# Performance work log

Hardware: AMD Instinct MI355X
Metric: run time of the kernel (lower is better)

The kernel has to match this reference:

```python
import jax, jax.numpy as jnp
import numpy as np

NUM_USERS = 100000
NUM_FEATURES = 1024
FACTORS = 64
B = 16384
TOTAL_FEATS = 524288  # B * 32 avg features per (user,item) pair


def setup_inputs() -> dict:
    key = jax.random.key(0)
    k1, k2, k3, k4, k5, k6 = jax.random.split(key, 6)
    user = jax.random.randint(k1, (B,), 0, NUM_USERS)
    # flattened ragged uifm[user][item] feature lists: sample_idx maps each
    # gathered feature id back to its batch row
    sample_idx = jax.random.randint(k2, (TOTAL_FEATS,), 0, B)
    feat_idx = jax.random.randint(k3, (TOTAL_FEATS,), 0, NUM_FEATURES)
    H = jax.random.normal(k4, (NUM_USERS, FACTORS), dtype=jnp.float32)
    G = jax.random.normal(k5, (NUM_FEATURES, FACTORS), dtype=jnp.float32)
    K = jax.random.normal(k6, (NUM_USERS, NUM_FEATURES), dtype=jnp.float32)
    return {"user": user, "sample_idx": sample_idx, "feat_idx": feat_idx,
            "H": H, "G": G, "K": K}


def reference(user, sample_idx, feat_idx, H, G, K):
    h_u = H[user]                      # [B, factors]
    z_u = jnp.einsum('bf,nf->bn', h_u, G)  # [B, num_features]
    a_u = K[user] * z_u                # [B, num_features] feature affinities
    # ragged gather-sum over per-(user,item) feature lists, then batch sum
    vals = a_u[sample_idx, feat_idx]   # [TOTAL_FEATS]
    return jnp.sum(vals)
```

## Files before the change

kernel.cpp:

```cpp
#include <hip/hip_runtime.h>

#define N_TOTAL   524288
#define B_ROWS    16384
#define FACTORS   64
#define NFEAT     1024

#define BM 128
#define BF 128
#define LDS_PAD 132

__global__ void zero_out_kernel(float* out) {
    out[0] = 0.0f;
}

__global__ __launch_bounds__(256, 2) void dense_c_kernel(
    const int*   __restrict__ user,
    const float* __restrict__ H,
    const float* __restrict__ G,
    float*       __restrict__ C,
    float*       __restrict__ out)
{
    if (blockIdx.x == 0 && threadIdx.x == 0) out[0] = 0.0f;

    __shared__ float sHT[FACTORS * LDS_PAD];
    __shared__ float sGT[FACTORS * LDS_PAD];

    const int t  = threadIdx.x;
    const int bb = (int)(blockIdx.x >> 3) * BM;
    const int bf = (int)(blockIdx.x & 7)  * BF;

    for (int i = t; i < BM * (FACTORS / 4); i += 256) {
        const int row  = i >> 4;
        const int slot = i & 15;

        const int u = user[bb + row];
        const float4 h = *(const float4*)(H + (long)u * FACTORS + slot * 4);
        sHT[(slot * 4 + 0) * LDS_PAD + row] = h.x;
        sHT[(slot * 4 + 1) * LDS_PAD + row] = h.y;
        sHT[(slot * 4 + 2) * LDS_PAD + row] = h.z;
        sHT[(slot * 4 + 3) * LDS_PAD + row] = h.w;

        const float4 g = *(const float4*)(G + (long)(bf + row) * FACTORS + slot * 4);
        sGT[(slot * 4 + 0) * LDS_PAD + row] = g.x;
        sGT[(slot * 4 + 1) * LDS_PAD + row] = g.y;
        sGT[(slot * 4 + 2) * LDS_PAD + row] = g.z;
        sGT[(slot * 4 + 3) * LDS_PAD + row] = g.w;
    }
    __syncthreads();

    const int tb = (t >> 4) * 8;
    const int tf = (t & 15) * 8;

    float acc[8][8] = {};

    #pragma unroll 4
    for (int k = 0; k < FACTORS; ++k) {
        float a[8], bv[8];
        *(float4*)&a[0]  = *(const float4*)&sHT[k * LDS_PAD + tb];
        *(float4*)&a[4]  = *(const float4*)&sHT[k * LDS_PAD + tb + 4];
        *(float4*)&bv[0] = *(const float4*)&sGT[k * LDS_PAD + tf];
        *(float4*)&bv[4] = *(const float4*)&sGT[k * LDS_PAD + tf + 4];
        #pragma unroll
        for (int i = 0; i < 8; ++i)
            #pragma unroll
            for (int j = 0; j < 8; ++j)
                acc[i][j] = fmaf(a[i], bv[j], acc[i][j]);
    }

    #pragma unroll
    for (int i = 0; i < 8; ++i) {
        float* cp = C + (long)(bb + tb + i) * NFEAT + (bf + tf);
        *(float4*)(cp)     = make_float4(acc[i][0], acc[i][1],
                                         acc[i][2], acc[i][3]);
        *(float4*)(cp + 4) = make_float4(acc[i][4], acc[i][5],
                                         acc[i][6], acc[i][7]);
    }
}

__global__ __launch_bounds__(256) void gather_sum_kernel(
    const int*   __restrict__ user,
    const int*   __restrict__ sample_idx,
    const int*   __restrict__ feat_idx,
    const float* __restrict__ K,
    const float* __restrict__ C,
    float*       __restrict__ out)
{
    const int base = (blockIdx.x * 256 + threadIdx.x) * 2;

    const int2 bs = *(const int2*)(sample_idx + base);
    const int2 fs = *(const int2*)(feat_idx + base);
    const int  u0 = user[bs.x];
    const int  u1 = user[bs.y];

    const float k0 = __builtin_nontemporal_load(K + (long)u0 * NFEAT + fs.x);
    const float k1 = __builtin_nontemporal_load(K + (long)u1 * NFEAT + fs.y);
    const float c0 = C[(long)bs.x * NFEAT + fs.x];
    const float c1 = C[(long)bs.y * NFEAT + fs.y];

    float local = fmaf(k0, c0, k1 * c1);

    #pragma unroll
    for (int off = 32; off > 0; off >>= 1)
        local += __shfl_down(local, off, 64);

    __shared__ float smem[4];
    const int lane = threadIdx.x & 63;
    const int wave = threadIdx.x >> 6;
    if (lane == 0) smem[wave] = local;
    __syncthreads();

    if (threadIdx.x == 0)
        atomicAdd(out, smem[0] + smem[1] + smem[2] + smem[3]);
}

__global__ __launch_bounds__(256) void kgflex_gather_kernel(
    const int*   __restrict__ user,
    const int*   __restrict__ sample_idx,
    const int*   __restrict__ feat_idx,
    const float* __restrict__ H,
    const float* __restrict__ G,
    const float* __restrict__ K,
    float*       __restrict__ out)
{
    const int tid    = blockIdx.x * blockDim.x + threadIdx.x;
    const int stride = gridDim.x * blockDim.x;

    float local = 0.0f;
    for (int i = tid; i < N_TOTAL; i += stride) {
        const int b = sample_idx[i];
        const int f = feat_idx[i];
        const int u = user[b];
        const float4* hp = (const float4*)(H + (long)u * FACTORS);
        const float4* gp = (const float4*)(G + (long)f * FACTORS);
        float acc = 0.0f;
        #pragma unroll
        for (int k = 0; k < FACTORS / 4; ++k) {
            const float4 h = hp[k];
            const float4 g = gp[k];
            acc += h.x * g.x + h.y * g.y + h.z * g.z + h.w * g.w;
        }
        local += K[(long)u * NFEAT + f] * acc;
    }
    #pragma unroll
    for (int off = 32; off > 0; off >>= 1)
        local += __shfl_down(local, off, 64);
    __shared__ float smem[4];
    const int lane = threadIdx.x & 63;
    const int wave = threadIdx.x >> 6;
    if (lane == 0) smem[wave] = local;
    __syncthreads();
    if (threadIdx.x == 0)
        atomicAdd(out, smem[0] + smem[1] + smem[2] + smem[3]);
}

extern "C" void kernel_launch(void* const* d_in, const int* in_sizes, int n_in,
                              void* d_out, int out_size, void* d_ws, size_t ws_size,
                              hipStream_t stream) {
    const int*   user       = (const int*)d_in[0];
    const int*   sample_idx = (const int*)d_in[1];
    const int*   feat_idx   = (const int*)d_in[2];
    const float* H          = (const float*)d_in[3];
    const float* G          = (const float*)d_in[4];
    const float* K          = (const float*)d_in[5];
    float* out = (float*)d_out;

    const size_t c_bytes = (size_t)B_ROWS * NFEAT * sizeof(float);

    if (ws_size >= c_bytes) {
        float* C = (float*)d_ws;
        dense_c_kernel<<<(B_ROWS / BM) * (NFEAT / BF), 256, 0, stream>>>(
            user, H, G, C, out);
        gather_sum_kernel<<<N_TOTAL / (256 * 2), 256, 0, stream>>>(
            user, sample_idx, feat_idx, K, C, out);
    } else {
        zero_out_kernel<<<1, 1, 0, stream>>>(out);
        kgflex_gather_kernel<<<2048, 256, 0, stream>>>(
            user, sample_idx, feat_idx, H, G, K, out);
    }
}
```

Baseline: 518.0 us.

## Replace dense C matmul with cooperative per-element gather dot products

The dense B×NFEAT matrix C is no longer computed and stored in workspace. Each element's 64-wide dot product H[u]·G[f] is now computed directly, with 16 lanes sharing one dot product through coalesced float4 loads and a shuffle reduction, two elements per quarter-wave per iteration. This removes the 64 MB write and read of C and the GEMM, at the cost of gathering H and G rows for every one of the 524288 elements. The old fallback kernel, which ran one thread per element, is replaced by this cooperative one.

```diff
diff --git a/kernel.cpp b/kernel.cpp
--- a/kernel.cpp
+++ b/kernel.cpp
@@ -1,119 +1,15 @@
 #include <hip/hip_runtime.h>
 
 #define N_TOTAL   524288
-#define B_ROWS    16384
 #define FACTORS   64
 #define NFEAT     1024
 
-#define BM 128
-#define BF 128
-#define LDS_PAD 132
 
 __global__ void zero_out_kernel(float* out) {
     out[0] = 0.0f;
 }
 
-__global__ __launch_bounds__(256, 2) void dense_c_kernel(
-    const int*   __restrict__ user,
-    const float* __restrict__ H,
-    const float* __restrict__ G,
-    float*       __restrict__ C,
-    float*       __restrict__ out)
-{
-    if (blockIdx.x == 0 && threadIdx.x == 0) out[0] = 0.0f;
-
-    __shared__ float sHT[FACTORS * LDS_PAD];
-    __shared__ float sGT[FACTORS * LDS_PAD];
-
-    const int t  = threadIdx.x;
-    const int bb = (int)(blockIdx.x >> 3) * BM;
-    const int bf = (int)(blockIdx.x & 7)  * BF;
-
-    for (int i = t; i < BM * (FACTORS / 4); i += 256) {
-        const int row  = i >> 4;
-        const int slot = i & 15;
-
-        const int u = user[bb + row];
-        const float4 h = *(const float4*)(H + (long)u * FACTORS + slot * 4);
-        sHT[(slot * 4 + 0) * LDS_PAD + row] = h.x;
-        sHT[(slot * 4 + 1) * LDS_PAD + row] = h.y;
-        sHT[(slot * 4 + 2) * LDS_PAD + row] = h.z;
-        sHT[(slot * 4 + 3) * LDS_PAD + row] = h.w;
-
-        const float4 g = *(const float4*)(G + (long)(bf + row) * FACTORS + slot * 4);
-        sGT[(slot * 4 + 0) * LDS_PAD + row] = g.x;
-        sGT[(slot * 4 + 1) * LDS_PAD + row] = g.y;
-        sGT[(slot * 4 + 2) * LDS_PAD + row] = g.z;
-        sGT[(slot * 4 + 3) * LDS_PAD + row] = g.w;
-    }
-    __syncthreads();
-
-    const int tb = (t >> 4) * 8;
-    const int tf = (t & 15) * 8;
-
-    float acc[8][8] = {};
-
-    #pragma unroll 4
-    for (int k = 0; k < FACTORS; ++k) {
-        float a[8], bv[8];
-        *(float4*)&a[0]  = *(const float4*)&sHT[k * LDS_PAD + tb];
-        *(float4*)&a[4]  = *(const float4*)&sHT[k * LDS_PAD + tb + 4];
-        *(float4*)&bv[0] = *(const float4*)&sGT[k * LDS_PAD + tf];
-        *(float4*)&bv[4] = *(const float4*)&sGT[k * LDS_PAD + tf + 4];
-        #pragma unroll
-        for (int i = 0; i < 8; ++i)
-            #pragma unroll
-            for (int j = 0; j < 8; ++j)
-                acc[i][j] = fmaf(a[i], bv[j], acc[i][j]);
-    }
-
-    #pragma unroll
-    for (int i = 0; i < 8; ++i) {
-        float* cp = C + (long)(bb + tb + i) * NFEAT + (bf + tf);
-        *(float4*)(cp)     = make_float4(acc[i][0], acc[i][1],
-                                         acc[i][2], acc[i][3]);
-        *(float4*)(cp + 4) = make_float4(acc[i][4], acc[i][5],
-                                         acc[i][6], acc[i][7]);
-    }
-}
-
-__global__ __launch_bounds__(256) void gather_sum_kernel(
-    const int*   __restrict__ user,
-    const int*   __restrict__ sample_idx,
-    const int*   __restrict__ feat_idx,
-    const float* __restrict__ K,
-    const float* __restrict__ C,
-    float*       __restrict__ out)
-{
-    const int base = (blockIdx.x * 256 + threadIdx.x) * 2;
-
-    const int2 bs = *(const int2*)(sample_idx + base);
-    const int2 fs = *(const int2*)(feat_idx + base);
-    const int  u0 = user[bs.x];
-    const int  u1 = user[bs.y];
-
-    const float k0 = __builtin_nontemporal_load(K + (long)u0 * NFEAT + fs.x);
-    const float k1 = __builtin_nontemporal_load(K + (long)u1 * NFEAT + fs.y);
-    const float c0 = C[(long)bs.x * NFEAT + fs.x];
-    const float c1 = C[(long)bs.y * NFEAT + fs.y];
-
-    float local = fmaf(k0, c0, k1 * c1);
-
-    #pragma unroll
-    for (int off = 32; off > 0; off >>= 1)
-        local += __shfl_down(local, off, 64);
-
-    __shared__ float smem[4];
-    const int lane = threadIdx.x & 63;
-    const int wave = threadIdx.x >> 6;
-    if (lane == 0) smem[wave] = local;
-    __syncthreads();
-
-    if (threadIdx.x == 0)
-        atomicAdd(out, smem[0] + smem[1] + smem[2] + smem[3]);
-}
-
-__global__ __launch_bounds__(256) void kgflex_gather_kernel(
+__global__ __launch_bounds__(256) void coop_gather_kernel(
     const int*   __restrict__ user,
     const int*   __restrict__ sample_idx,
     const int*   __restrict__ feat_idx,
@@ -122,33 +18,55 @@
     const float* __restrict__ K,
     float*       __restrict__ out)
 {
-    const int tid    = blockIdx.x * blockDim.x + threadIdx.x;
-    const int stride = gridDim.x * blockDim.x;
+    const int lane = threadIdx.x & 63;
+    const int sub  = lane >> 4;
+    const int slot = lane & 15;
+
+    const int wid    = (blockIdx.x * 256 + threadIdx.x) >> 6;
+    const int nwaves = (gridDim.x * 256) >> 6;
 
     float local = 0.0f;
-    for (int i = tid; i < N_TOTAL; i += stride) {
-        const int b = sample_idx[i];
-        const int f = feat_idx[i];
-        const int u = user[b];
-        const float4* hp = (const float4*)(H + (long)u * FACTORS);
-        const float4* gp = (const float4*)(G + (long)f * FACTORS);
-        float acc = 0.0f;
-        #pragma unroll
-        for (int k = 0; k < FACTORS / 4; ++k) {
-            const float4 h = hp[k];
-            const float4 g = gp[k];
-            acc += h.x * g.x + h.y * g.y + h.z * g.z + h.w * g.w;
+
+    for (int e8 = wid * 8; e8 < N_TOTAL; e8 += nwaves * 8) {
+        const int eA = e8 + sub;
+        const int eB = e8 + 4 + sub;
+
+        const int bA = sample_idx[eA];
+        const int bB = sample_idx[eB];
+        const int fA = feat_idx[eA];
+        const int fB = feat_idx[eB];
+        const int uA = user[bA];
+        const int uB = user[bB];
+
+        const float4 hA = *(const float4*)(H + (long)uA * FACTORS + slot * 4);
+        const float4 gA = *(const float4*)(G + (long)fA * FACTORS + slot * 4);
+        const float4 hB = *(const float4*)(H + (long)uB * FACTORS + slot * 4);
+        const float4 gB = *(const float4*)(G + (long)fB * FACTORS + slot * 4);
+
+        float dA = hA.x * gA.x + hA.y * gA.y + hA.z * gA.z + hA.w * gA.w;
+        float dB = hB.x * gB.x + hB.y * gB.y + hB.z * gB.z + hB.w * gB.w;
+
+        dA += __shfl_xor(dA, 8, 64);  dB += __shfl_xor(dB, 8, 64);
+        dA += __shfl_xor(dA, 4, 64);  dB += __shfl_xor(dB, 4, 64);
+        dA += __shfl_xor(dA, 2, 64);  dB += __shfl_xor(dB, 2, 64);
+        dA += __shfl_xor(dA, 1, 64);  dB += __shfl_xor(dB, 1, 64);
+
+        if (slot == 0) {
+            const float kA = __builtin_nontemporal_load(K + (long)uA * NFEAT + fA);
+            const float kB = __builtin_nontemporal_load(K + (long)uB * NFEAT + fB);
+            local += kA * dA + kB * dB;
         }
-        local += K[(long)u * NFEAT + f] * acc;
     }
+
     #pragma unroll
     for (int off = 32; off > 0; off >>= 1)
         local += __shfl_down(local, off, 64);
+
     __shared__ float smem[4];
-    const int lane = threadIdx.x & 63;
     const int wave = threadIdx.x >> 6;
     if (lane == 0) smem[wave] = local;
     __syncthreads();
+
     if (threadIdx.x == 0)
         atomicAdd(out, smem[0] + smem[1] + smem[2] + smem[3]);
 }
@@ -164,17 +82,8 @@
     const float* K          = (const float*)d_in[5];
     float* out = (float*)d_out;
 
-    const size_t c_bytes = (size_t)B_ROWS * NFEAT * sizeof(float);
+    zero_out_kernel<<<1, 1, 0, stream>>>(out);
 
-    if (ws_size >= c_bytes) {
-        float* C = (float*)d_ws;
-        dense_c_kernel<<<(B_ROWS / BM) * (NFEAT / BF), 256, 0, stream>>>(
-            user, H, G, C, out);
-        gather_sum_kernel<<<N_TOTAL / (256 * 2), 256, 0, stream>>>(
-            user, sample_idx, feat_idx, K, C, out);
-    } else {
-        zero_out_kernel<<<1, 1, 0, stream>>>(out);
-        kgflex_gather_kernel<<<2048, 256, 0, stream>>>(
-            user, sample_idx, feat_idx, H, G, K, out);
-    }
+    coop_gather_kernel<<<1024, 256, 0, stream>>>(
+        user, sample_idx, feat_idx, H, G, K, out);
 }
```

Result: faster. 497.1 us (-4.0%).
